# Optimization experiments

Measured on AMD Instinct MI355X. Metric: run time of the kernel, lower is better.

## Reference

```python
import jax, jax.numpy as jnp
import numpy as np

N_NODES = 100000


def setup_inputs() -> dict:
    key = jax.random.key(0)
    ks = jax.random.split(key, 4)
    x = jax.random.normal(ks[0], (N_NODES, 64), dtype=jnp.float32)
    edge_index = jax.random.randint(ks[1], (2, 1600000), 0, N_NODES, dtype=jnp.int64)
    # Glorot-ish scaled weights
    W1 = jax.random.normal(ks[2], (64, 64), dtype=jnp.float32) * (1.0 / np.sqrt(64))
    b1 = jnp.zeros((64,), dtype=jnp.float32)
    W2 = jax.random.normal(ks[3], (64, 19), dtype=jnp.float32) * (1.0 / np.sqrt(64))
    b2 = jnp.zeros((19,), dtype=jnp.float32)
    return {"x": x, "edge_index": edge_index, "W1": W1, "b1": b1, "W2": W2, "b2": b2}


def _gcn_norm(edge_index, num_nodes, dtype):
    # PyG gcn_norm: add self-loops (fill_value=1, improved=False), then
    # norm = deg^-1/2[src] * deg^-1/2[dst] with deg computed over destination.
    loops = jnp.arange(num_nodes, dtype=edge_index.dtype)
    src = jnp.concatenate([edge_index[0], loops])
    dst = jnp.concatenate([edge_index[1], loops])
    deg = jax.ops.segment_sum(jnp.ones_like(dst, dtype=dtype), dst, num_segments=num_nodes)
    dinv = jax.lax.rsqrt(deg)  # deg >= 1 thanks to self-loops
    norm = dinv[src] * dinv[dst]  # [E + N]
    return src, dst, norm


def _gcn_conv(h, src, dst, norm, W, b, num_nodes):
    hw = h @ W                                  # dense transform [N, d_out]
    msg = norm[:, None] * hw[src]               # gather + edge scaling [E+N, d_out]
    out = jax.ops.segment_sum(msg, dst, num_segments=num_nodes)  # scatter-add
    return out + b


def reference(x, edge_index, W1, b1, W2, b2):
    n = x.shape[0]
    src, dst, norm = _gcn_norm(edge_index, n, x.dtype)
    h = jax.nn.relu(_gcn_conv(x, src, dst, norm, W1, b1, n))
    # dropout is identity in eval mode (training=False)
    return _gcn_conv(h, src, dst, norm, W2, b2, n)
```

## Files before the change

kernel.cpp:

```cpp
#include <hip/hip_runtime.h>

#define TPB 256
#define BSH 5
#define BNODES 32
#define CAP 1024
#define EPB 4096
#define NBMAX 3200


__global__ void k_hist1(const int* __restrict__ dst, int* __restrict__ hist,
                        int nb, int E) {
    __shared__ int sh[NBMAX];
    int tid = threadIdx.x, blk = blockIdx.x;
    for (int i = tid; i < nb; i += TPB) sh[i] = 0;
    __syncthreads();
    int e0 = blk * EPB;
    for (int i = tid; i < EPB; i += TPB) {
        int e = e0 + i;
        if (e < E) atomicAdd(&sh[dst[e] >> BSH], 1);
    }
    __syncthreads();
    int* hrow = hist + (size_t)blk * nb;
    for (int i = tid; i < nb; i += TPB) hrow[i] = sh[i];
}

__global__ void k_scanoff(const int* __restrict__ hist, int* __restrict__ offs,
                          int* __restrict__ bcnt, int nblk, int nb) {
    int t = blockIdx.x * TPB + threadIdx.x;
    int b = t >> 3, s = t & 7;
    if (b >= nb) return;
    int nps = (nblk + 7) >> 3;
    int sum = 0;
    for (int q = 0; q < nps; ++q) {
        int blk = q * 8 + s;
        if (blk < nblk) sum += hist[(size_t)blk * nb + b];
    }
    int v = sum;
#pragma unroll
    for (int o = 1; o < 8; o <<= 1) {
        int u = __shfl_up(v, o, 8);
        if (s >= o) v += u;
    }
    int total = __shfl(v, 7, 8);
    if (s == 0) bcnt[b] = total;
    int off = b * CAP + (v - sum);
    for (int q = 0; q < nps; ++q) {
        int blk = q * 8 + s;
        if (blk < nblk) {
            offs[(size_t)blk * nb + b] = off;
            off += hist[(size_t)blk * nb + b];
        }
    }
}

__global__ void k_scatter(const int* __restrict__ src, const int* __restrict__ dst,
                          const int* __restrict__ offs, unsigned* __restrict__ ebuf,
                          int nb, int E) {
    __shared__ int cur[NBMAX];
    int tid = threadIdx.x, blk = blockIdx.x;
    const int* orow = offs + (size_t)blk * nb;
    for (int i = tid; i < nb; i += TPB) cur[i] = orow[i];
    __syncthreads();
    int e0 = blk * EPB;
    for (int i = tid; i < EPB; i += TPB) {
        int e = e0 + i;
        if (e < E) {
            int d = dst[e];
            int pos = atomicAdd(&cur[d >> BSH], 1);
            ebuf[pos] = ((unsigned)src[e] << BSH) | (unsigned)(d & (BNODES - 1));
        }
    }
}

__global__ void k_bcsr(const int* __restrict__ bcnt, const unsigned* __restrict__ ebuf,
                       int* __restrict__ csr, int* __restrict__ node_beg,
                       int* __restrict__ degi, float* __restrict__ dinv, int nb, int n) {
    __shared__ unsigned se[4][CAP];
    __shared__ int scnt[4][BNODES];
    __shared__ int sexc[4][BNODES];
    __shared__ int srnk[4][BNODES];
    int wv = threadIdx.x >> 6, lane = threadIdx.x & 63;
    int b = blockIdx.x * 4 + wv;
    bool act = (b < nb);
    if (lane < BNODES) { scnt[wv][lane] = 0; srnk[wv][lane] = 0; }
    __syncthreads();
    int cnt = 0;
    if (act) {
        cnt = bcnt[b];
        if (cnt > CAP) cnt = CAP;
        const unsigned* p = &ebuf[(size_t)b * CAP];
        for (int k = lane; k < cnt; k += 64) {
            unsigned pk = p[k];
            se[wv][k] = pk;
            atomicAdd(&scnt[wv][pk & (BNODES - 1)], 1);
        }
    }
    __syncthreads();
    if (act && lane < BNODES) {
        int dg = scnt[wv][lane];
        int v = dg;
#pragma unroll
        for (int off = 1; off < BNODES; off <<= 1) {
            int t = __shfl_up(v, off, BNODES);
            if (lane >= off) v += t;
        }
        int excl = v - dg;
        sexc[wv][lane] = excl;
        int node = b * BNODES + lane;
        if (node < n) {
            degi[node] = dg;
            node_beg[node] = b * CAP + excl;
            dinv[node] = rsqrtf((float)dg + 1.0f);
        }
    }
    __syncthreads();
    if (act) {
        int* csrb = csr + (size_t)b * CAP;
        for (int k = lane; k < cnt; k += 64) {
            unsigned pk = se[wv][k];
            int dl = pk & (BNODES - 1);
            int r = atomicAdd(&srnk[wv][dl], 1);
            csrb[sexc[wv][dl] + r] = (int)(pk >> BSH);
        }
    }
}


__global__ void k_xw64v(const float* __restrict__ x, const float* __restrict__ W,
                        const float* __restrict__ dinv, _Float16* __restrict__ g, int n) {
    __shared__ float Ws[64 * 64];
    __shared__ float xsT[64 * 64];
    int tid = threadIdx.x;
    int row0 = blockIdx.x * 64;
    for (int i = tid; i < 1024; i += TPB)
        reinterpret_cast<float4*>(Ws)[i] = reinterpret_cast<const float4*>(W)[i];
    {
        int rl = tid >> 2, cq = (tid & 3) * 16;
        int row = row0 + rl;
#pragma unroll
        for (int j4 = 0; j4 < 4; ++j4) {
            float4 v = make_float4(0.f, 0.f, 0.f, 0.f);
            if (row < n) v = *reinterpret_cast<const float4*>(x + (size_t)row * 64 + cq + j4 * 4);
            xsT[(cq + j4 * 4 + 0) * 64 + rl] = v.x;
            xsT[(cq + j4 * 4 + 1) * 64 + rl] = v.y;
            xsT[(cq + j4 * 4 + 2) * 64 + rl] = v.z;
            xsT[(cq + j4 * 4 + 3) * 64 + rl] = v.w;
        }
    }
    __syncthreads();
    int c4 = (tid & 15) * 4, rq = (tid >> 4) * 4;
    float acc[4][4] = {};
#pragma unroll 4
    for (int k = 0; k < 64; ++k) {
        float4 wv = *reinterpret_cast<const float4*>(Ws + k * 64 + c4);
        float4 xv = *reinterpret_cast<const float4*>(xsT + k * 64 + rq);
        const float* wp = (const float*)&wv;
        const float* xp = (const float*)&xv;
#pragma unroll
        for (int i = 0; i < 4; ++i)
#pragma unroll
            for (int j = 0; j < 4; ++j) acc[i][j] += xp[i] * wp[j];
    }
#pragma unroll
    for (int i = 0; i < 4; ++i) {
        int row = row0 + rq + i;
        if (row < n) {
            float dv = dinv[row];
            _Float16 o[4];
#pragma unroll
            for (int j = 0; j < 4; ++j) o[j] = (_Float16)(dv * acc[i][j]);
            *reinterpret_cast<ushort4*>(g + (size_t)row * 64 + c4) =
                *reinterpret_cast<const ushort4*>(o);
        }
    }
}

__global__ void k_xw19v(const _Float16* __restrict__ h, const float* __restrict__ W,
                        const float* __restrict__ dinv, _Float16* __restrict__ g2, int n) {
    __shared__ float Ws[64 * 32];
    __shared__ float xsT[64 * 32];
    int tid = threadIdx.x;
    int row0 = blockIdx.x * 32;
    for (int i = tid; i < 64 * 32; i += TPB) {
        int k = i >> 5, c = i & 31;
        Ws[i] = (c < 19) ? W[k * 19 + c] : 0.f;
    }
    {
        int rl = tid >> 3, sq = tid & 7;
        int row = row0 + rl;
        if (row < n) {
            uint4 v = *(reinterpret_cast<const uint4*>(h + (size_t)row * 64) + sq);
            const _Float16* f = (const _Float16*)&v;
#pragma unroll
            for (int j = 0; j < 8; ++j) xsT[(sq * 8 + j) * 32 + rl] = (float)f[j];
        } else {
#pragma unroll
            for (int j = 0; j < 8; ++j) xsT[(sq * 8 + j) * 32 + rl] = 0.f;
        }
    }
    __syncthreads();
    int c = tid & 31, rg = (tid >> 5) * 4;
    float acc[4] = {};
#pragma unroll 4
    for (int k = 0; k < 64; ++k) {
        float wv = Ws[k * 32 + c];
        float4 xv = *reinterpret_cast<const float4*>(xsT + k * 32 + rg);
        const float* xp = (const float*)&xv;
#pragma unroll
        for (int i = 0; i < 4; ++i) acc[i] += xp[i] * wv;
    }
    if (c < 19) {
#pragma unroll
        for (int i = 0; i < 4; ++i) {
            int row = row0 + rg + i;
            if (row < n) g2[(size_t)row * 19 + c] = (_Float16)(dinv[row] * acc[i]);
        }
    }
}


__global__ void k_gath64d(const int* __restrict__ node_beg, const int* __restrict__ degi,
                          const int* __restrict__ csr, const float* __restrict__ dinv,
                          const _Float16* __restrict__ g, const float* __restrict__ b1,
                          _Float16* __restrict__ h, int n) {
    int node = blockIdx.x * 4 + (threadIdx.x >> 6);
    if (node >= n) return;
    int lane = threadIdx.x & 63;
    int eidx = lane >> 3, fch = lane & 7;
    int beg = node_beg[node], cnt = degi[node];
    const uint4* gb = (const uint4*)g;
    float acc[8];
#pragma unroll
    for (int j = 0; j < 8; ++j) acc[j] = 0.f;
    for (int base = 0; base < cnt; base += 16) {
        int ka = base + eidx, kb = base + 8 + eidx;
        bool va = (ka < cnt), vb = (kb < cnt);
        int ra = va ? csr[beg + ka] : 0;
        int rb = vb ? csr[beg + kb] : 0;
        uint4 A = va ? gb[(size_t)ra * 8 + fch] : make_uint4(0, 0, 0, 0);
        uint4 B = vb ? gb[(size_t)rb * 8 + fch] : make_uint4(0, 0, 0, 0);
        const _Float16* fa = (const _Float16*)&A;
        const _Float16* fb = (const _Float16*)&B;
#pragma unroll
        for (int j = 0; j < 8; ++j) acc[j] += (float)fa[j] + (float)fb[j];
    }
#pragma unroll
    for (int m = 8; m < 64; m <<= 1) {
#pragma unroll
        for (int j = 0; j < 8; ++j) acc[j] += __shfl_xor(acc[j], m);
    }
    if (eidx == 0) {
        uint4 v = gb[(size_t)node * 8 + fch];
        const _Float16* f = (const _Float16*)&v;
        float dv = dinv[node];
        _Float16 outv[8];
#pragma unroll
        for (int j = 0; j < 8; ++j) {
            float val = dv * (acc[j] + (float)f[j]) + b1[fch * 8 + j];
            outv[j] = (_Float16)fmaxf(val, 0.f);
        }
        *((uint4*)(h + (size_t)node * 64) + fch) = *(const uint4*)outv;
    }
}

__global__ void k_gath19(const int* __restrict__ node_beg, const int* __restrict__ degi,
                         const int* __restrict__ csr, const float* __restrict__ dinv,
                         const _Float16* __restrict__ g2, const float* __restrict__ b2,
                         float* __restrict__ out, int n) {
    int node = blockIdx.x * 8 + (threadIdx.x >> 5);
    if (node >= n) return;
    int c = threadIdx.x & 31;
    if (c >= 19) return;
    int beg = node_beg[node], cnt = degi[node];
    float a0 = (float)g2[(size_t)node * 19 + c];
    float a1 = 0.f, a2 = 0.f, a3 = 0.f;
    float a4 = 0.f, a5 = 0.f, a6 = 0.f, a7 = 0.f;
    int k = 0;
    for (; k + 7 < cnt; k += 8) {
        int s0 = csr[beg + k];
        int s1 = csr[beg + k + 1];
        int s2 = csr[beg + k + 2];
        int s3 = csr[beg + k + 3];
        int s4 = csr[beg + k + 4];
        int s5 = csr[beg + k + 5];
        int s6 = csr[beg + k + 6];
        int s7 = csr[beg + k + 7];
        a0 += (float)g2[(size_t)s0 * 19 + c];
        a1 += (float)g2[(size_t)s1 * 19 + c];
        a2 += (float)g2[(size_t)s2 * 19 + c];
        a3 += (float)g2[(size_t)s3 * 19 + c];
        a4 += (float)g2[(size_t)s4 * 19 + c];
        a5 += (float)g2[(size_t)s5 * 19 + c];
        a6 += (float)g2[(size_t)s6 * 19 + c];
        a7 += (float)g2[(size_t)s7 * 19 + c];
    }
    for (; k < cnt; ++k) a1 += (float)g2[(size_t)csr[beg + k] * 19 + c];
    float s = ((a0 + a1) + (a2 + a3)) + ((a4 + a5) + (a6 + a7));
    out[(size_t)node * 19 + c] = dinv[node] * s + b2[c];
}


extern "C" void kernel_launch(void* const* d_in, const int* in_sizes, int n_in,
                              void* d_out, int out_size, void* d_ws, size_t ws_size,
                              hipStream_t stream) {
    const float* x  = (const float*)d_in[0];
    const int*   ei = (const int*)d_in[1];
    const float* W1 = (const float*)d_in[2];
    const float* b1 = (const float*)d_in[3];
    const float* W2 = (const float*)d_in[4];
    const float* b2 = (const float*)d_in[5];
    float* out = (float*)d_out;

    int N = in_sizes[0] / 64;
    int E = in_sizes[1] / 2;
    const int* src = ei;
    const int* dst = ei + E;

    int NB = (N + BNODES - 1) >> BSH;
    int NBLK = (E + EPB - 1) / EPB;

    char* w = (char*)d_ws;
    int* bcnt      = (int*)w;      w += (size_t)NB * 4;
    int* degi      = (int*)w;      w += (size_t)N * 4;
    int* node_beg  = (int*)w;      w += (size_t)N * 4;
    float* dinv    = (float*)w;    w += (size_t)N * 4;
    w = (char*)(((size_t)w + 63) & ~(size_t)63);
    char* regionA  = w;
    size_t histB   = (size_t)NBLK * NB * 4;
    size_t csrB    = (size_t)NB * CAP * 4;
    size_t regA    = (histB * 2 > csrB) ? histB * 2 : csrB;
    int* hist      = (int*)regionA;
    int* offs      = (int*)(regionA + histB);
    int* csr       = (int*)regionA;
    w += regA;
    unsigned* ebuf = (unsigned*)w; w += (size_t)NB * CAP * 4;
    _Float16* g1   = (_Float16*)w; w += (size_t)N * 64 * 2;
    _Float16* h    = (_Float16*)w; w += (size_t)N * 64 * 2;
    _Float16* g2   = g1;

    k_hist1   <<<NBLK, TPB, 0, stream>>>(dst, hist, NB, E);
    k_scanoff <<<(NB * 8 + TPB - 1) / TPB, TPB, 0, stream>>>(hist, offs, bcnt, NBLK, NB);
    k_scatter <<<NBLK, TPB, 0, stream>>>(src, dst, offs, ebuf, NB, E);
    k_bcsr    <<<(NB + 3) / 4, TPB, 0, stream>>>(bcnt, ebuf, csr, node_beg, degi, dinv, NB, N);

    k_xw64v   <<<(N + 63) / 64, TPB, 0, stream>>>(x, W1, dinv, g1, N);
    k_gath64d <<<(N + 3) / 4, TPB, 0, stream>>>(node_beg, degi, csr, dinv, g1, b1, h, N);

    k_xw19v   <<<(N + 31) / 32, TPB, 0, stream>>>(h, W2, dinv, g2, N);
    k_gath19  <<<(N + 7) / 8, TPB, 0, stream>>>(node_beg, degi, csr, dinv, g2, b2, out, N);
}
```

Baseline: 194.4 us.

## Fuse layer-1 aggregation with layer-2 dense transform into one kernel

Merges the 64-wide gather/ReLU kernel with the 64x19 matmul, so each node's hidden vector stays in registers and is multiplied by W2 staged in shared memory. A shuffle reduction then produces the 19 scaled outputs. This removes a kernel launch and the write and re-read of the N x 64 half-precision hidden buffer. It also widens the gather loop to four neighbours per lane per iteration for more memory-level parallelism. In exchange every block reloads W2 into shared memory and does the extra per-node shuffle work.

```diff
diff --git a/kernel.cpp b/kernel.cpp
--- a/kernel.cpp
+++ b/kernel.cpp
@@ -175,91 +175,81 @@
     }
 }
 
-__global__ void k_xw19v(const _Float16* __restrict__ h, const float* __restrict__ W,
-                        const float* __restrict__ dinv, _Float16* __restrict__ g2, int n) {
-    __shared__ float Ws[64 * 32];
-    __shared__ float xsT[64 * 32];
+
+__global__ void k_g64f(const int* __restrict__ node_beg, const int* __restrict__ degi,
+                       const int* __restrict__ csr, const float* __restrict__ dinv,
+                       const _Float16* __restrict__ g, const float* __restrict__ b1,
+                       const float* __restrict__ W2, _Float16* __restrict__ g2, int n) {
+    __shared__ float W2s[64 * 19];
+    __shared__ float b1s[64];
     int tid = threadIdx.x;
-    int row0 = blockIdx.x * 32;
-    for (int i = tid; i < 64 * 32; i += TPB) {
-        int k = i >> 5, c = i & 31;
-        Ws[i] = (c < 19) ? W[k * 19 + c] : 0.f;
-    }
-    {
-        int rl = tid >> 3, sq = tid & 7;
-        int row = row0 + rl;
-        if (row < n) {
-            uint4 v = *(reinterpret_cast<const uint4*>(h + (size_t)row * 64) + sq);
-            const _Float16* f = (const _Float16*)&v;
-#pragma unroll
-            for (int j = 0; j < 8; ++j) xsT[(sq * 8 + j) * 32 + rl] = (float)f[j];
-        } else {
-#pragma unroll
-            for (int j = 0; j < 8; ++j) xsT[(sq * 8 + j) * 32 + rl] = 0.f;
-        }
-    }
-    __syncthreads();
-    int c = tid & 31, rg = (tid >> 5) * 4;
-    float acc[4] = {};
-#pragma unroll 4
-    for (int k = 0; k < 64; ++k) {
-        float wv = Ws[k * 32 + c];
-        float4 xv = *reinterpret_cast<const float4*>(xsT + k * 32 + rg);
-        const float* xp = (const float*)&xv;
-#pragma unroll
-        for (int i = 0; i < 4; ++i) acc[i] += xp[i] * wv;
-    }
-    if (c < 19) {
-#pragma unroll
-        for (int i = 0; i < 4; ++i) {
-            int row = row0 + rg + i;
-            if (row < n) g2[(size_t)row * 19 + c] = (_Float16)(dinv[row] * acc[i]);
-        }
-    }
-}
-
-
-__global__ void k_gath64d(const int* __restrict__ node_beg, const int* __restrict__ degi,
-                          const int* __restrict__ csr, const float* __restrict__ dinv,
-                          const _Float16* __restrict__ g, const float* __restrict__ b1,
-                          _Float16* __restrict__ h, int n) {
-    int node = blockIdx.x * 4 + (threadIdx.x >> 6);
+    for (int i = tid; i < 64 * 19; i += TPB) W2s[i] = W2[i];
+    if (tid < 64) b1s[tid] = b1[tid];
+    __syncthreads();
+
+    int node = blockIdx.x * 4 + (tid >> 6);
     if (node >= n) return;
-    int lane = threadIdx.x & 63;
+    int lane = tid & 63;
     int eidx = lane >> 3, fch = lane & 7;
     int beg = node_beg[node], cnt = degi[node];
     const uint4* gb = (const uint4*)g;
     float acc[8];
 #pragma unroll
     for (int j = 0; j < 8; ++j) acc[j] = 0.f;
-    for (int base = 0; base < cnt; base += 16) {
-        int ka = base + eidx, kb = base + 8 + eidx;
-        bool va = (ka < cnt), vb = (kb < cnt);
-        int ra = va ? csr[beg + ka] : 0;
-        int rb = vb ? csr[beg + kb] : 0;
-        uint4 A = va ? gb[(size_t)ra * 8 + fch] : make_uint4(0, 0, 0, 0);
-        uint4 B = vb ? gb[(size_t)rb * 8 + fch] : make_uint4(0, 0, 0, 0);
+    for (int base = 0; base < cnt; base += 32) {
+        int k0 = base + eidx, k1 = base + 8 + eidx;
+        int k2 = base + 16 + eidx, k3 = base + 24 + eidx;
+        bool v0 = (k0 < cnt), v1 = (k1 < cnt), v2 = (k2 < cnt), v3 = (k3 < cnt);
+        int r0 = v0 ? csr[beg + k0] : 0;
+        int r1 = v1 ? csr[beg + k1] : 0;
+        int r2 = v2 ? csr[beg + k2] : 0;
+        int r3 = v3 ? csr[beg + k3] : 0;
+        uint4 A = v0 ? gb[(size_t)r0 * 8 + fch] : make_uint4(0, 0, 0, 0);
+        uint4 B = v1 ? gb[(size_t)r1 * 8 + fch] : make_uint4(0, 0, 0, 0);
+        uint4 C = v2 ? gb[(size_t)r2 * 8 + fch] : make_uint4(0, 0, 0, 0);
+        uint4 D = v3 ? gb[(size_t)r3 * 8 + fch] : make_uint4(0, 0, 0, 0);
         const _Float16* fa = (const _Float16*)&A;
         const _Float16* fb = (const _Float16*)&B;
-#pragma unroll
-        for (int j = 0; j < 8; ++j) acc[j] += (float)fa[j] + (float)fb[j];
+        const _Float16* fc = (const _Float16*)&C;
+        const _Float16* fd = (const _Float16*)&D;
+#pragma unroll
+        for (int j = 0; j < 8; ++j)
+            acc[j] += ((float)fa[j] + (float)fb[j]) + ((float)fc[j] + (float)fd[j]);
     }
 #pragma unroll
     for (int m = 8; m < 64; m <<= 1) {
 #pragma unroll
         for (int j = 0; j < 8; ++j) acc[j] += __shfl_xor(acc[j], m);
     }
-    if (eidx == 0) {
-        uint4 v = gb[(size_t)node * 8 + fch];
-        const _Float16* f = (const _Float16*)&v;
-        float dv = dinv[node];
-        _Float16 outv[8];
+    uint4 sv = gb[(size_t)node * 8 + fch];
+    const _Float16* sf = (const _Float16*)&sv;
+    float dv = dinv[node];
+    float hv[8];
+#pragma unroll
+    for (int j = 0; j < 8; ++j)
+        hv[j] = fmaxf(dv * (acc[j] + (float)sf[j]) + b1s[fch * 8 + j], 0.f);
+    float p0 = 0.f, p1 = 0.f, p2 = 0.f;
+    {
+        int c0 = eidx, c1 = eidx + 8, c2 = eidx + 16;
 #pragma unroll
         for (int j = 0; j < 8; ++j) {
-            float val = dv * (acc[j] + (float)f[j]) + b1[fch * 8 + j];
-            outv[j] = (_Float16)fmaxf(val, 0.f);
-        }
-        *((uint4*)(h + (size_t)node * 64) + fch) = *(const uint4*)outv;
+            float hj = hv[j];
+            const float* wrow = W2s + (fch * 8 + j) * 19;
+            p0 += hj * wrow[c0];
+            p1 += hj * wrow[c1];
+            if (c2 < 19) p2 += hj * wrow[c2];
+        }
+    }
+#pragma unroll
+    for (int m = 1; m < 8; m <<= 1) {
+        p0 += __shfl_xor(p0, m);
+        p1 += __shfl_xor(p1, m);
+        p2 += __shfl_xor(p2, m);
+    }
+    if (fch == 0) {
+        g2[(size_t)node * 19 + eidx] = (_Float16)(dv * p0);
+        g2[(size_t)node * 19 + eidx + 8] = (_Float16)(dv * p1);
+        if (eidx + 16 < 19) g2[(size_t)node * 19 + eidx + 16] = (_Float16)(dv * p2);
     }
 }
 
@@ -335,8 +325,7 @@
     w += regA;
     unsigned* ebuf = (unsigned*)w; w += (size_t)NB * CAP * 4;
     _Float16* g1   = (_Float16*)w; w += (size_t)N * 64 * 2;
-    _Float16* h    = (_Float16*)w; w += (size_t)N * 64 * 2;
-    _Float16* g2   = g1;
+    _Float16* g2   = (_Float16*)w; w += (size_t)N * 19 * 2;
 
     k_hist1   <<<NBLK, TPB, 0, stream>>>(dst, hist, NB, E);
     k_scanoff <<<(NB * 8 + TPB - 1) / TPB, TPB, 0, stream>>>(hist, offs, bcnt, NBLK, NB);
@@ -344,8 +333,6 @@
     k_bcsr    <<<(NB + 3) / 4, TPB, 0, stream>>>(bcnt, ebuf, csr, node_beg, degi, dinv, NB, N);
 
     k_xw64v   <<<(N + 63) / 64, TPB, 0, stream>>>(x, W1, dinv, g1, N);
-    k_gath64d <<<(N + 3) / 4, TPB, 0, stream>>>(node_beg, degi, csr, dinv, g1, b1, h, N);
-
-    k_xw19v   <<<(N + 31) / 32, TPB, 0, stream>>>(h, W2, dinv, g2, N);
+    k_g64f    <<<(N + 3) / 4, TPB, 0, stream>>>(node_beg, degi, csr, dinv, g1, b1, W2, g2, N);
     k_gath19  <<<(N + 7) / 8, TPB, 0, stream>>>(node_beg, degi, csr, dinv, g2, b2, out, N);
 }
```

Result: slower. 200.3 us (+3.1%).
